# Kernel tuning notes

Measured on AMD Instinct MI355X. Metric: run time of the kernel, lower is better.

The kernel has to match this reference:

```python
import jax, jax.numpy as jnp
import numpy as np

NUM_CLASSES = 100
EPS = 1e-8  # torch F.cosine_similarity default eps


def setup_inputs() -> dict:
    key = jax.random.key(0)
    k1, k2 = jax.random.split(key)
    feat = jax.random.normal(k1, (100000, 512), dtype=jnp.float32)
    label = jax.random.randint(k2, (100000,), 0, NUM_CLASSES, dtype=jnp.int64)
    return {"feat": feat, "label": label}


def reference(feat, label):
    # Per-class mean (segment mean) -- replaces the Python loop over classes.
    sums = jax.ops.segment_sum(feat, label, num_segments=NUM_CLASSES)          # [C, D]
    counts = jax.ops.segment_sum(jnp.ones_like(label, dtype=feat.dtype), label,
                                 num_segments=NUM_CLASSES)                      # [C]
    means = sums / jnp.maximum(counts, 1.0)[:, None]                            # [C, D]

    # Only the gathered (own-class) column of the sim matrix is returned,
    # so compute cos(feat[i], means[label[i]]) directly.
    cent = means[label]                                                         # [N, D]
    dot = jnp.sum(feat * cent, axis=-1)                                         # [N]
    n_feat = jnp.maximum(jnp.linalg.norm(feat, axis=-1), EPS)
    n_cent = jnp.maximum(jnp.linalg.norm(cent, axis=-1), EPS)
    return dot / (n_feat * n_cent)
```

## Files before the change

### kernel.cpp

```cpp
#include <hip/hip_runtime.h>

#define NCLS 100
#define DIM  512
#define EPSV 1e-8f

#define DSPL   4
#define CH     192
#define BATCH  16

__global__ __launch_bounds__(256) void hist_kernel(const int* __restrict__ label,
                                                   int* __restrict__ cnt, int n) {
    __shared__ int h[NCLS];
    for (int i = threadIdx.x; i < NCLS; i += 256) h[i] = 0;
    __syncthreads();
    for (int i = blockIdx.x * 256 + threadIdx.x; i < n; i += gridDim.x * 256)
        atomicAdd(&h[label[i]], 1);
    __syncthreads();
    for (int i = threadIdx.x; i < NCLS; i += 256) {
        int v = h[i];
        if (v) atomicAdd(&cnt[i], v);
    }
}

__global__ __launch_bounds__(64) void sum_kernel(const float* __restrict__ feat,
                                                 const int* __restrict__ label,
                                                 float* __restrict__ partial, int n) {
    __shared__ float acc[NCLS * 128];
    const int lane = threadIdx.x;
    const int ds   = blockIdx.x;
    const int ch   = blockIdx.y;

    #pragma unroll 4
    for (int i = lane; i < NCLS * 128; i += 64) acc[i] = 0.0f;

    const int rpc  = (n + CH - 1) / CH;
    const int r0   = ch * rpc;
    const int rows = min(rpc, n - r0);
    const float* fb = feat + (size_t)ds * 128 + (size_t)lane * 2;
    float2* accv = (float2*)acc;

    int r = 0;
    for (; r + BATCH <= rows; r += BATCH) {
        float2 v[BATCH];
        int    c[BATCH];
        #pragma unroll
        for (int k = 0; k < BATCH; ++k) {
            c[k] = label[r0 + r + k];
            v[k] = *(const float2*)(fb + (size_t)(r0 + r + k) * DIM);
        }
        #pragma unroll
        for (int i = 0; i < BATCH; ++i) {
            #pragma unroll
            for (int j = i + 1; j < BATCH; ++j) {
                if (c[j] == c[i]) { v[i].x += v[j].x; v[i].y += v[j].y; c[j] = -1; }
            }
        }
        float2 t[BATCH];
        #pragma unroll
        for (int k = 0; k < BATCH; ++k)
            if (c[k] >= 0) t[k] = accv[c[k] * 64 + lane];
        #pragma unroll
        for (int k = 0; k < BATCH; ++k)
            if (c[k] >= 0) {
                t[k].x += v[k].x; t[k].y += v[k].y;
                accv[c[k] * 64 + lane] = t[k];
            }
    }
    for (; r < rows; ++r) {
        const int c0 = label[r0 + r];
        float2 v = *(const float2*)(fb + (size_t)(r0 + r) * DIM);
        float2 t = accv[c0 * 64 + lane];
        t.x += v.x; t.y += v.y;
        accv[c0 * 64 + lane] = t;
    }

    float* dst = partial + ((size_t)ch * DSPL + ds) * (NCLS * 128);
    #pragma unroll 4
    for (int i = lane; i < NCLS * 128; i += 64) dst[i] = acc[i];
}

__global__ __launch_bounds__(512) void finalize_kernel(const float* __restrict__ partial,
                                                       const int* __restrict__ cnt,
                                                       float* __restrict__ mhat) {
    const int c = blockIdx.x;
    const int t = threadIdx.x;
    const int ds  = t >> 7;
    const int off = t & 127;
    const float* p = partial + ((size_t)ds * NCLS + c) * 128 + off;
    const size_t stride = (size_t)DSPL * NCLS * 128;

    float a0 = 0.f, a1 = 0.f, a2 = 0.f, a3 = 0.f;
    for (int ch = 0; ch < CH; ch += 4) {
        a0 += p[(size_t)(ch + 0) * stride];
        a1 += p[(size_t)(ch + 1) * stride];
        a2 += p[(size_t)(ch + 2) * stride];
        a3 += p[(size_t)(ch + 3) * stride];
    }
    const float m = ((a0 + a1) + (a2 + a3)) / fmaxf((float)cnt[c], 1.0f);

    float ss = m * m;
    #pragma unroll
    for (int o = 32; o; o >>= 1) ss += __shfl_down(ss, o, 64);
    __shared__ float red[8];
    if ((t & 63) == 0) red[t >> 6] = ss;
    __syncthreads();
    float tot = 0.f;
    #pragma unroll
    for (int k = 0; k < 8; ++k) tot += red[k];
    const float q = 1.0f / fmaxf(sqrtf(tot), EPSV);
    mhat[(size_t)c * DIM + t] = m * q;
}

__global__ __launch_bounds__(256) void cos_kernel(const float* __restrict__ feat,
                                                  const int* __restrict__ label,
                                                  const float* __restrict__ mhat,
                                                  float* __restrict__ out, int n) {
    const int lane = threadIdx.x & 63;
    const int wv   = threadIdx.x >> 6;
    const int cl   = lane >> 4;
    const int t    = lane & 15;

    const int row = blockIdx.x * 16 + wv * 4 + cl;
    const bool ok = row < n;
    const int rr = ok ? row : (n - 1);

    const int c = label[rr];
    const float4* f4 = (const float4*)(feat + (size_t)rr * DIM);
    const float4* m4 = (const float4*)(mhat + (size_t)c  * DIM);

    float4 a[8], b[8];
    #pragma unroll
    for (int j = 0; j < 8; ++j) a[j] = f4[t + 16 * j];
    #pragma unroll
    for (int j = 0; j < 8; ++j) b[j] = m4[t + 16 * j];

    float dot = 0.0f, nf = 0.0f;
    #pragma unroll
    for (int j = 0; j < 8; ++j) {
        dot += a[j].x * b[j].x + a[j].y * b[j].y + a[j].z * b[j].z + a[j].w * b[j].w;
        nf  += a[j].x * a[j].x + a[j].y * a[j].y + a[j].z * a[j].z + a[j].w * a[j].w;
    }

    #pragma unroll
    for (int off = 8; off; off >>= 1) {
        dot += __shfl_xor(dot, off, 64);
        nf  += __shfl_xor(nf,  off, 64);
    }
    if (t == 0 && ok) {
        out[row] = dot / fmaxf(sqrtf(nf), EPSV);
    }
}

extern "C" void kernel_launch(void* const* d_in, const int* in_sizes, int n_in,
                              void* d_out, int out_size, void* d_ws, size_t ws_size,
                              hipStream_t stream) {
    const float* feat  = (const float*)d_in[0];
    const int*   label = (const int*)d_in[1];
    float*       out   = (float*)d_out;
    const int n = in_sizes[0] / DIM;

    int*   cnt     = (int*)d_ws;
    float* mhat    = (float*)(cnt + 128);
    float* partial = mhat + NCLS * DIM;

    hipMemsetAsync(cnt, 0, 128 * sizeof(int), stream);

    hist_kernel<<<160, 256, 0, stream>>>(label, cnt, n);

    dim3 sg(DSPL, CH);
    sum_kernel<<<sg, 64, 0, stream>>>(feat, label, partial, n);

    finalize_kernel<<<NCLS, 512, 0, stream>>>(partial, cnt, mhat);

    cos_kernel<<<(n + 15) / 16, 256, 0, stream>>>(feat, label, mhat, out, n);
}
```

Before: 401.3 us.

## Restructure segment-sum kernel with double-buffered loads and shuffle-broadcast labels

The segment-sum kernel now splits the feature dimension 8 ways, so each lane owns one float column, and the row batch grows to 32. Two register buffers hold alternating batches so the next batch's global loads are in flight while the current one is merged into shared memory. Each lane loads one label and the rest are broadcast with shuffles. Duplicate labels are merged branch-free within sub-groups of 8, and merged rows are redirected to a dummy shared row. The aim is to hide global-load latency and cut shared-memory traffic, at the cost of more registers, twice as many blocks, and more partial reads in finalize.

```diff
diff --git a/kernel.cpp b/kernel.cpp
--- a/kernel.cpp
+++ b/kernel.cpp
@@ -4,9 +4,10 @@
 #define DIM  512
 #define EPSV 1e-8f
 
-#define DSPL   4
+#define DSPL   8
 #define CH     192
-#define BATCH  16
+#define BATCH  32
+#define SUBG   8
 
 __global__ __launch_bounds__(256) void hist_kernel(const int* __restrict__ label,
                                                    int* __restrict__ cnt, int n) {
@@ -25,58 +26,76 @@
 __global__ __launch_bounds__(64) void sum_kernel(const float* __restrict__ feat,
                                                  const int* __restrict__ label,
                                                  float* __restrict__ partial, int n) {
-    __shared__ float acc[NCLS * 128];
+    __shared__ float acc[(NCLS + 1) * 64];
     const int lane = threadIdx.x;
     const int ds   = blockIdx.x;
     const int ch   = blockIdx.y;
 
-    #pragma unroll 4
-    for (int i = lane; i < NCLS * 128; i += 64) acc[i] = 0.0f;
+    float4* a4 = (float4*)acc;
+    #pragma unroll
+    for (int i = lane; i < (NCLS + 1) * 16; i += 64)
+        a4[i] = make_float4(0.f, 0.f, 0.f, 0.f);
 
     const int rpc  = (n + CH - 1) / CH;
     const int r0   = ch * rpc;
     const int rows = min(rpc, n - r0);
-    const float* fb = feat + (size_t)ds * 128 + (size_t)lane * 2;
-    float2* accv = (float2*)acc;
+    const float* fb = feat + ds * 64 + lane;
 
-    int r = 0;
-    for (; r + BATCH <= rows; r += BATCH) {
-        float2 v[BATCH];
-        int    c[BATCH];
-        #pragma unroll
-        for (int k = 0; k < BATCH; ++k) {
-            c[k] = label[r0 + r + k];
-            v[k] = *(const float2*)(fb + (size_t)(r0 + r + k) * DIM);
-        }
-        #pragma unroll
-        for (int i = 0; i < BATCH; ++i) {
-            #pragma unroll
-            for (int j = i + 1; j < BATCH; ++j) {
-                if (c[j] == c[i]) { v[i].x += v[j].x; v[i].y += v[j].y; c[j] = -1; }
-            }
-        }
-        float2 t[BATCH];
+    float vA[BATCH], vB[BATCH];
+    int mylA = 0, mylB = 0;
+
+    auto loadA = [&](int rb) {
+        mylA = label[r0 + rb + (lane & (BATCH - 1))];
         #pragma unroll
         for (int k = 0; k < BATCH; ++k)
-            if (c[k] >= 0) t[k] = accv[c[k] * 64 + lane];
+            vA[k] = fb[(size_t)(r0 + rb + k) * DIM];
+    };
+    auto loadB = [&](int rb) {
+        mylB = label[r0 + rb + (lane & (BATCH - 1))];
         #pragma unroll
         for (int k = 0; k < BATCH; ++k)
-            if (c[k] >= 0) {
-                t[k].x += v[k].x; t[k].y += v[k].y;
-                accv[c[k] * 64 + lane] = t[k];
+            vB[k] = fb[(size_t)(r0 + rb + k) * DIM];
+    };
+    auto proc = [&](int myl, float (&v)[BATCH]) {
+        int c[BATCH];
+        #pragma unroll
+        for (int k = 0; k < BATCH; ++k) c[k] = __shfl(myl, k, 64);
+        #pragma unroll
+        for (int g = 0; g < BATCH; g += SUBG) {
+            #pragma unroll
+            for (int i = 0; i < SUBG; ++i) {
+                #pragma unroll
+                for (int j = i + 1; j < SUBG; ++j) {
+                    const bool eq = (c[g + j] == c[g + i]);
+                    v[g + i] += eq ? v[g + j] : 0.0f;
+                    c[g + j] = eq ? NCLS : c[g + j];
+                }
             }
+            float t[SUBG];
+            #pragma unroll
+            for (int k = 0; k < SUBG; ++k) t[k] = acc[c[g + k] * 64 + lane];
+            #pragma unroll
+            for (int k = 0; k < SUBG; ++k) acc[c[g + k] * 64 + lane] = t[k] + v[g + k];
+        }
+    };
+
+    const int nb = rows / BATCH;
+    if (nb > 0) {
+        loadA(0);
+        for (int ib = 0; ib + 1 < nb; ++ib) {
+            if (ib & 1) { loadA((ib + 1) * BATCH); proc(mylB, vB); }
+            else        { loadB((ib + 1) * BATCH); proc(mylA, vA); }
+        }
+        if ((nb - 1) & 1) proc(mylB, vB); else proc(mylA, vA);
     }
-    for (; r < rows; ++r) {
+    for (int r = nb * BATCH; r < rows; ++r) {
         const int c0 = label[r0 + r];
-        float2 v = *(const float2*)(fb + (size_t)(r0 + r) * DIM);
-        float2 t = accv[c0 * 64 + lane];
-        t.x += v.x; t.y += v.y;
-        accv[c0 * 64 + lane] = t;
+        acc[c0 * 64 + lane] += fb[(size_t)(r0 + r) * DIM];
     }
 
-    float* dst = partial + ((size_t)ch * DSPL + ds) * (NCLS * 128);
-    #pragma unroll 4
-    for (int i = lane; i < NCLS * 128; i += 64) dst[i] = acc[i];
+    float4* dst = (float4*)(partial + ((size_t)ch * DSPL + ds) * (NCLS * 64));
+    #pragma unroll
+    for (int i = lane; i < NCLS * 16; i += 64) dst[i] = a4[i];
 }
 
 __global__ __launch_bounds__(512) void finalize_kernel(const float* __restrict__ partial,
@@ -84,10 +103,10 @@
                                                        float* __restrict__ mhat) {
     const int c = blockIdx.x;
     const int t = threadIdx.x;
-    const int ds  = t >> 7;
-    const int off = t & 127;
-    const float* p = partial + ((size_t)ds * NCLS + c) * 128 + off;
-    const size_t stride = (size_t)DSPL * NCLS * 128;
+    const int ds  = t >> 6;
+    const int off = t & 63;
+    const float* p = partial + (size_t)ds * (NCLS * 64) + (size_t)c * 64 + off;
+    const size_t stride = (size_t)DSPL * NCLS * 64;
 
     float a0 = 0.f, a1 = 0.f, a2 = 0.f, a3 = 0.f;
     for (int ch = 0; ch < CH; ch += 4) {
```

Measured after the change: 354.5 us. 1.13x faster.

## Use fixed-point LDS integer atomics for segment sums and fold histogram in

Applied to the files above, without the earlier changes.

Replaces the per-wave batched duplicate-merging float accumulation with fixed-point integer atomicAdd into LDS, using 4 waves per block and 8 dimension splits. Class counts are now computed inside the sum kernel by one column of blocks, which removes the separate histogram kernel and the memset. The finalize step sums the int partials in 64-bit and rescales them. This trades exact float accumulation for quantization at a 2^18 scale, and int32 LDS accumulators could overflow for large values.

```diff
diff --git a/kernel.cpp b/kernel.cpp
--- a/kernel.cpp
+++ b/kernel.cpp
@@ -4,104 +4,109 @@
 #define DIM  512
 #define EPSV 1e-8f
 
-#define DSPL   4
-#define CH     192
-#define BATCH  16
+#define DSPL 8
+#define CH   192
+#define NW   4
+#define SCALE    262144.0f
+#define INVSCALE (1.0f / 262144.0f)
 
-__global__ __launch_bounds__(256) void hist_kernel(const int* __restrict__ label,
-                                                   int* __restrict__ cnt, int n) {
-    __shared__ int h[NCLS];
-    for (int i = threadIdx.x; i < NCLS; i += 256) h[i] = 0;
+__global__ __launch_bounds__(256) void sum_kernel(const float* __restrict__ feat,
+                                                  const int* __restrict__ label,
+                                                  int* __restrict__ partial,
+                                                  int* __restrict__ cntp, int n) {
+    __shared__ int acc[NCLS * 64];
+    __shared__ int hcnt[NCLS];
+    const int tid = threadIdx.x;
+    const int ds  = blockIdx.x;
+    const int ch  = blockIdx.y;
+
+    for (int i = tid; i < NCLS * 64; i += 256) acc[i] = 0;
+    if (ds == 0)
+        for (int i = tid; i < NCLS; i += 256) hcnt[i] = 0;
     __syncthreads();
-    for (int i = blockIdx.x * 256 + threadIdx.x; i < n; i += gridDim.x * 256)
-        atomicAdd(&h[label[i]], 1);
-    __syncthreads();
-    for (int i = threadIdx.x; i < NCLS; i += 256) {
-        int v = h[i];
-        if (v) atomicAdd(&cnt[i], v);
-    }
-}
-
-__global__ __launch_bounds__(64) void sum_kernel(const float* __restrict__ feat,
-                                                 const int* __restrict__ label,
-                                                 float* __restrict__ partial, int n) {
-    __shared__ float acc[NCLS * 128];
-    const int lane = threadIdx.x;
-    const int ds   = blockIdx.x;
-    const int ch   = blockIdx.y;
-
-    #pragma unroll 4
-    for (int i = lane; i < NCLS * 128; i += 64) acc[i] = 0.0f;
 
     const int rpc  = (n + CH - 1) / CH;
     const int r0   = ch * rpc;
-    const int rows = min(rpc, n - r0);
-    const float* fb = feat + (size_t)ds * 128 + (size_t)lane * 2;
-    float2* accv = (float2*)acc;
+    const int rows = max(0, min(rpc, n - r0));
+    const int w    = tid >> 6;
+    const int lane = tid & 63;
+    const int lo   = (rows * w) / NW;
+    const int hi   = (rows * (w + 1)) / NW;
+    const float* fb = feat + ds * 64 + lane;
 
-    int r = 0;
-    for (; r + BATCH <= rows; r += BATCH) {
-        float2 v[BATCH];
-        int    c[BATCH];
+    int r = lo;
+    for (; r + 8 <= hi; r += 8) {
+        float v[8];
         #pragma unroll
-        for (int k = 0; k < BATCH; ++k) {
-            c[k] = label[r0 + r + k];
-            v[k] = *(const float2*)(fb + (size_t)(r0 + r + k) * DIM);
+        for (int k = 0; k < 8; ++k) v[k] = fb[(size_t)(r0 + r + k) * DIM];
+        const int myl = label[r0 + r + (lane & 7)];
+        int c[8];
+        #pragma unroll
+        for (int k = 0; k < 8; ++k) c[k] = __shfl(myl, k, 64);
+
+        #pragma unroll
+        for (int k = 0; k < 8; ++k)
+            atomicAdd(&acc[c[k] * 64 + lane], __float2int_rn(v[k] * SCALE));
+        if (ds == 0 && lane == 0) {
+            #pragma unroll
+            for (int k = 0; k < 8; ++k) atomicAdd(&hcnt[c[k]], 1);
         }
-        #pragma unroll
-        for (int i = 0; i < BATCH; ++i) {
-            #pragma unroll
-            for (int j = i + 1; j < BATCH; ++j) {
-                if (c[j] == c[i]) { v[i].x += v[j].x; v[i].y += v[j].y; c[j] = -1; }
-            }
-        }
-        float2 t[BATCH];
-        #pragma unroll
-        for (int k = 0; k < BATCH; ++k)
-            if (c[k] >= 0) t[k] = accv[c[k] * 64 + lane];
-        #pragma unroll
-        for (int k = 0; k < BATCH; ++k)
-            if (c[k] >= 0) {
-                t[k].x += v[k].x; t[k].y += v[k].y;
-                accv[c[k] * 64 + lane] = t[k];
-            }
     }
-    for (; r < rows; ++r) {
-        const int c0 = label[r0 + r];
-        float2 v = *(const float2*)(fb + (size_t)(r0 + r) * DIM);
-        float2 t = accv[c0 * 64 + lane];
-        t.x += v.x; t.y += v.y;
-        accv[c0 * 64 + lane] = t;
+    for (; r < hi; ++r) {
+        const float v = fb[(size_t)(r0 + r) * DIM];
+        const int   c = label[r0 + r];
+        atomicAdd(&acc[c * 64 + lane], __float2int_rn(v * SCALE));
+        if (ds == 0 && lane == 0) atomicAdd(&hcnt[c], 1);
     }
+    __syncthreads();
 
-    float* dst = partial + ((size_t)ch * DSPL + ds) * (NCLS * 128);
-    #pragma unroll 4
-    for (int i = lane; i < NCLS * 128; i += 64) dst[i] = acc[i];
+    int4* d4 = (int4*)(partial + ((size_t)ch * DSPL + ds) * (NCLS * 64));
+    const int4* s4 = (const int4*)acc;
+    for (int i = tid; i < NCLS * 16; i += 256) d4[i] = s4[i];
+    if (ds == 0)
+        for (int i = tid; i < NCLS; i += 256) cntp[ch * 128 + i] = hcnt[i];
 }
 
-__global__ __launch_bounds__(512) void finalize_kernel(const float* __restrict__ partial,
-                                                       const int* __restrict__ cnt,
+__global__ __launch_bounds__(512) void finalize_kernel(const int* __restrict__ partial,
+                                                       const int* __restrict__ cntp,
                                                        float* __restrict__ mhat) {
     const int c = blockIdx.x;
     const int t = threadIdx.x;
-    const int ds  = t >> 7;
-    const int off = t & 127;
-    const float* p = partial + ((size_t)ds * NCLS + c) * 128 + off;
-    const size_t stride = (size_t)DSPL * NCLS * 128;
+    __shared__ int   csh[8];
+    __shared__ float red[8];
+    __shared__ float invsh;
 
-    float a0 = 0.f, a1 = 0.f, a2 = 0.f, a3 = 0.f;
+    int pc = 0;
+    for (int ch = t; ch < CH; ch += 512) pc += cntp[ch * 128 + c];
+    #pragma unroll
+    for (int o = 32; o; o >>= 1) pc += __shfl_down(pc, o, 64);
+    if ((t & 63) == 0) csh[t >> 6] = pc;
+    __syncthreads();
+    if (t == 0) {
+        int tot = 0;
+        #pragma unroll
+        for (int k = 0; k < 8; ++k) tot += csh[k];
+        invsh = INVSCALE / fmaxf((float)tot, 1.0f);
+    }
+    __syncthreads();
+    const float inv = invsh;
+
+    const int ds  = t >> 6;
+    const int off = t & 63;
+    const int* p = partial + ((size_t)ds * NCLS + c) * 64 + off;
+    const size_t stride = (size_t)DSPL * NCLS * 64;
+    long long a0 = 0, a1 = 0, a2 = 0, a3 = 0;
     for (int ch = 0; ch < CH; ch += 4) {
         a0 += p[(size_t)(ch + 0) * stride];
         a1 += p[(size_t)(ch + 1) * stride];
         a2 += p[(size_t)(ch + 2) * stride];
         a3 += p[(size_t)(ch + 3) * stride];
     }
-    const float m = ((a0 + a1) + (a2 + a3)) / fmaxf((float)cnt[c], 1.0f);
+    const float m = (float)((a0 + a1) + (a2 + a3)) * inv;
 
     float ss = m * m;
     #pragma unroll
     for (int o = 32; o; o >>= 1) ss += __shfl_down(ss, o, 64);
-    __shared__ float red[8];
     if ((t & 63) == 0) red[t >> 6] = ss;
     __syncthreads();
     float tot = 0.f;
@@ -159,18 +164,14 @@
     float*       out   = (float*)d_out;
     const int n = in_sizes[0] / DIM;
 
-    int*   cnt     = (int*)d_ws;
-    float* mhat    = (float*)(cnt + 128);
-    float* partial = mhat + NCLS * DIM;
-
-    hipMemsetAsync(cnt, 0, 128 * sizeof(int), stream);
-
-    hist_kernel<<<160, 256, 0, stream>>>(label, cnt, n);
+    float* mhat    = (float*)d_ws;
+    int*   cntp    = (int*)(mhat + NCLS * DIM);
+    int*   partial = cntp + CH * 128;
 
     dim3 sg(DSPL, CH);
-    sum_kernel<<<sg, 64, 0, stream>>>(feat, label, partial, n);
+    sum_kernel<<<sg, 256, 0, stream>>>(feat, label, partial, cntp, n);
 
-    finalize_kernel<<<NCLS, 512, 0, stream>>>(partial, cnt, mhat);
+    finalize_kernel<<<NCLS, 512, 0, stream>>>(partial, cntp, mhat);
 
     cos_kernel<<<(n + 15) / 16, 256, 0, stream>>>(feat, label, mhat, out, n);
 }
```

Result: faster. 332.2 us (-17.2%).
